# Optimization experiments

Hardware: AMD Instinct MI355X
Metric: run time of the kernel (lower is better)

The kernel has to match this reference:

```python
import jax, jax.numpy as jnp
import numpy as np

EPS = 1e-5

def layernorm(x, g, b):
    mu = jnp.mean(x, axis=-1, keepdims=True)
    var = jnp.mean((x - mu) ** 2, axis=-1, keepdims=True)
    return (x - mu) * jax.lax.rsqrt(var + EPS) * g + b

def setup_inputs() -> dict:
    key = jax.random.key(0)
    B, T, C, H = 4, 2048, 1024, 16
    hs = C // H  # 64
    ks = jax.random.split(key, 16)
    s_in = 1.0 / np.sqrt(C)
    s_hid = 1.0 / np.sqrt(4 * C)
    return {
        "x":   jax.random.normal(ks[0], (B, T, C), jnp.float32),
        # per-head projections, stacked over heads: [H, C, hs]
        "Wq":  jax.random.normal(ks[1], (H, C, hs), jnp.float32) * s_in,
        "Wk":  jax.random.normal(ks[2], (H, C, hs), jnp.float32) * s_in,
        "Wv":  jax.random.normal(ks[3], (H, C, hs), jnp.float32) * s_in,
        # output projection [C, C] (concat of heads -> C)
        "Wo":  jax.random.normal(ks[4], (C, C), jnp.float32) * s_in,
        "bo":  jnp.zeros((C,), jnp.float32),
        # layernorm params
        "g1":  jnp.ones((C,), jnp.float32),
        "be1": jnp.zeros((C,), jnp.float32),
        "g2":  jnp.ones((C,), jnp.float32),
        "be2": jnp.zeros((C,), jnp.float32),
        # feed-forward: C -> 4C -> C
        "W1":  jax.random.normal(ks[5], (C, 4 * C), jnp.float32) * s_in,
        "b1":  jnp.zeros((4 * C,), jnp.float32),
        "W2":  jax.random.normal(ks[6], (4 * C, C), jnp.float32) * s_hid,
        "b2":  jnp.zeros((C,), jnp.float32),
    }

def reference(x, Wq, Wk, Wv, Wo, bo, g1, be1, g2, be2, W1, b1, W2, b2):
    B, T, C = x.shape
    H, _, hs = Wq.shape
    scale = hs ** -0.5

    # --- self-attention on ln1(x) ---
    xn = layernorm(x, g1, be1)
    q = jnp.einsum('btc,hcd->bhtd', xn, Wq)
    k = jnp.einsum('btc,hcd->bhtd', xn, Wk)
    v = jnp.einsum('btc,hcd->bhtd', xn, Wv)
    scores = jnp.einsum('bhtd,bhsd->bhts', q, k) * scale  # [B,H,T,T]
    causal = jnp.tril(jnp.ones((T, T), dtype=bool))
    scores = jnp.where(causal, scores, jnp.finfo(scores.dtype).min)
    wei = jax.nn.softmax(scores, axis=-1)
    out = jnp.einsum('bhts,bhsd->bhtd', wei, v)           # [B,H,T,hs]
    out = out.transpose(0, 2, 1, 3).reshape(B, T, H * hs)  # concat heads
    x = x + out @ Wo + bo

    # --- feed-forward on ln2(x) ---
    xn2 = layernorm(x, g2, be2)
    h = jax.nn.relu(xn2 @ W1 + b1)
    x = x + h @ W2 + b2
    return x
```

## Files before the change

### kernel.cpp

```cpp
#include <hip/hip_runtime.h>
#include <hip/hip_bf16.h>

typedef __hip_bfloat16 bf16;
typedef __attribute__((ext_vector_type(8))) short bf16x8;
typedef __attribute__((ext_vector_type(4))) short s16x4;
typedef __attribute__((ext_vector_type(4))) float f32x4;
typedef __attribute__((ext_vector_type(16))) float f32x16;
typedef __attribute__((ext_vector_type(2))) unsigned int u32x2;
typedef __attribute__((ext_vector_type(4))) unsigned int u32x4;

__device__ __forceinline__ float b2f(bf16 v) { return __bfloat162float(v); }
__device__ __forceinline__ bf16  f2b(float v) { return __float2bfloat16(v); }
__device__ __forceinline__ float ldf(const bf16* p)  { return __bfloat162float(*p); }
__device__ __forceinline__ float ldf(const float* p) { return *p; }
__device__ __forceinline__ void  stf(bf16* p, float v)  { *p = __float2bfloat16(v); }
__device__ __forceinline__ void  stf(float* p, float v) { *p = v; }

__device__ __forceinline__ unsigned cvt_pk_bf16(float lo, float hi) {
    unsigned r;
    asm("v_cvt_pk_bf16_f32 %0, %1, %2" : "=v"(r) : "v"(lo), "v"(hi));
    return r;
}

__device__ __forceinline__ void ld4(const float* p, float* v) {
    float4 t = *(const float4*)p;
    v[0] = t.x; v[1] = t.y; v[2] = t.z; v[3] = t.w;
}
__device__ __forceinline__ void ld4(const bf16* p, float* v) {
    s16x4 t = *(const s16x4*)p;
#pragma unroll
    for (int j = 0; j < 4; ++j) { short s = t[j]; v[j] = b2f(*(bf16*)&s); }
}

__device__ __forceinline__ void load_lds16(const bf16* g, short* lds) {
    __builtin_amdgcn_global_load_lds(
        (const __attribute__((address_space(1))) unsigned int*)g,
        (__attribute__((address_space(3))) unsigned int*)lds, 16, 0, 0);
}

template<typename InT>
__global__ __launch_bounds__(256) void ln_kernel(const InT* __restrict__ x,
                                                 const float* __restrict__ g,
                                                 const float* __restrict__ b,
                                                 bf16* __restrict__ out)
{
    const int C = 1024;
    int row = blockIdx.x;
    int tid = threadIdx.x;
    const InT* xr = x + (size_t)row * C;

    float v[4];
    ld4(xr + tid * 4, v);
    float s = 0.f, s2 = 0.f;
#pragma unroll
    for (int i = 0; i < 4; ++i) { s += v[i]; s2 += v[i] * v[i]; }
#pragma unroll
    for (int off = 32; off > 0; off >>= 1) {
        s  += __shfl_down(s,  off, 64);
        s2 += __shfl_down(s2, off, 64);
    }
    __shared__ float red[8];
    int wave = tid >> 6;
    if ((tid & 63) == 0) { red[wave] = s; red[wave + 4] = s2; }
    __syncthreads();
    float ts  = red[0] + red[1] + red[2] + red[3];
    float ts2 = red[4] + red[5] + red[6] + red[7];
    float mu  = ts * (1.f / 1024.f);
    float var = ts2 * (1.f / 1024.f) - mu * mu;
    float rstd = rsqrtf(var + 1e-5f);

    float4 gg = *(const float4*)(g + tid * 4);
    float4 bb = *(const float4*)(b + tid * 4);
    float gj[4] = {gg.x, gg.y, gg.z, gg.w};
    float bj[4] = {bb.x, bb.y, bb.z, bb.w};
    s16x4 o4;
#pragma unroll
    for (int j = 0; j < 4; ++j) {
        bf16 ob = f2b((v[j] - mu) * rstd * gj[j] + bj[j]);
        o4[j] = *(short*)&ob;
    }
    *(s16x4*)(out + (size_t)row * C + tid * 4) = o4;
}

__global__ __launch_bounds__(256) void prep_weights(
    const float* __restrict__ Wq, const float* __restrict__ Wk,
    const float* __restrict__ Wv, const float* __restrict__ Wo,
    const float* __restrict__ W1, const float* __restrict__ W2,
    bf16* __restrict__ wqkvt, bf16* __restrict__ wot,
    bf16* __restrict__ w1t, bf16* __restrict__ w2t)
{
    __shared__ float t[32][33];
    int tx = threadIdx.x & 31, ty = threadIdx.x >> 5;
    int id = blockIdx.x;
    const float* in; bf16* out; int in_ld, out_ld, n0, k0;
    if (id < 3072) {
        const float* Ws[3] = {Wq, Wk, Wv};
        int m = id >> 10, r = id & 1023;
        int z = r >> 6, rt = r & 63;
        in = Ws[m] + z * 65536;
        out = wqkvt + (size_t)(m * 1024 + z * 64) * 1024;
        in_ld = 64; out_ld = 1024;
        n0 = (rt & 1) * 32; k0 = (rt >> 1) * 32;
    } else if (id < 4096) {
        int r = id - 3072;
        in = Wo; out = wot; in_ld = 1024; out_ld = 1024;
        n0 = (r & 31) * 32; k0 = (r >> 5) * 32;
    } else if (id < 8192) {
        int r = id - 4096;
        in = W1; out = w1t; in_ld = 4096; out_ld = 1024;
        n0 = (r & 127) * 32; k0 = (r >> 7) * 32;
    } else {
        int r = id - 8192;
        in = W2; out = w2t; in_ld = 1024; out_ld = 4096;
        n0 = (r & 31) * 32; k0 = (r >> 5) * 32;
    }
#pragma unroll
    for (int i = 0; i < 4; ++i)
        t[ty + i * 8][tx] = in[(size_t)(k0 + ty + i * 8) * in_ld + n0 + tx];
    __syncthreads();
#pragma unroll
    for (int i = 0; i < 4; ++i)
        out[(size_t)(n0 + ty + i * 8) * out_ld + k0 + tx] = f2b(t[tx][ty + i * 8]);
}

__global__ __launch_bounds__(256) void vt_kernel(
    const bf16* __restrict__ qkv, bf16* __restrict__ vt, int T)
{
    __shared__ float t[32][33];
    int tx = threadIdx.x & 31, ty = threadIdx.x >> 5;
    int z = blockIdx.z, b = z >> 4, h = z & 15;
    const bf16* in = qkv + (size_t)b * T * 3072 + 2048 + h * 64;
    bf16* out = vt + (size_t)z * 64 * T;
    int n0 = blockIdx.x * 32, k0 = blockIdx.y * 32;
#pragma unroll
    for (int i = 0; i < 4; ++i)
        t[ty + i * 8][tx] = b2f(in[(size_t)(k0 + ty + i * 8) * 3072 + n0 + tx]);
    __syncthreads();
#pragma unroll
    for (int i = 0; i < 4; ++i)
        out[(size_t)(n0 + ty + i * 8) * T + k0 + tx] = f2b(t[tx][ty + i * 8]);
}

template<bool RELU, bool HAS_BIAS, typename OutT>
__global__ __launch_bounds__(512, 2) void gemm8p(
    const bf16* __restrict__ A, int lda,
    const bf16* __restrict__ Bt, int ldb,
    const float* __restrict__ bias,
    OutT* __restrict__ Cm, int ldc,
    int M, int N, int K)
{
    __shared__ short As[4][8192];
    __shared__ short Bs[4][8192];
    int tid = threadIdx.x, wv = tid >> 6, ln = tid & 63;
    int quad = ln >> 4, lane15 = ln & 15;

    int nbn = N >> 8;
    int nwg = gridDim.x;
    int f2 = (blockIdx.x & 7) * (nwg >> 3) + (blockIdx.x >> 3);
    int by = f2 / nbn, bx = f2 % nbn;
    int bm0 = by << 8, bn0 = bx << 8;

    int wr = wv >> 2, wc = wv & 3;
    const int NT = K >> 5;

    int sr = tid >> 2;
    int sc = ((tid & 3) ^ ((sr >> 1) & 3)) * 8;
    const bf16* Ab1 = A  + (size_t)(bm0 + sr) * lda + sc;
    const bf16* Ab2 = A  + (size_t)(bm0 + 128 + sr) * lda + sc;
    const bf16* Bb1 = Bt + (size_t)(bn0 + sr) * ldb + sc;
    const bf16* Bb2 = Bt + (size_t)(bn0 + 128 + sr) * ldb + sc;

#define STAGE_A8(bf_, u_) { \
    load_lds16(Ab1 + (u_) * 32, &As[bf_][wv * 512]); \
    load_lds16(Ab2 + (u_) * 32, &As[bf_][4096 + wv * 512]); }
#define STAGE_B8(bf_, u_) { \
    load_lds16(Bb1 + (u_) * 32, &Bs[bf_][wv * 512]); \
    load_lds16(Bb2 + (u_) * 32, &Bs[bf_][4096 + wv * 512]); }

    f32x4 acc[8][4] = {};
    int arow = wr * 128 + lane15;
    int brow = wc * 64 + lane15;
    int sw = (quad ^ ((lane15 >> 1) & 3)) * 8;

    STAGE_A8(0, 0); STAGE_B8(0, 0);
    STAGE_A8(1, 1); STAGE_B8(1, 1);
    STAGE_A8(2, 2); STAGE_B8(2, 2);
    asm volatile("s_waitcnt vmcnt(8)" ::: "memory");
    __builtin_amdgcn_s_barrier();

    for (int t = 0; t < NT; ++t) {
        int buf = t & 3;
        const short* Al = &As[buf][0];
        const short* Bl = &Bs[buf][0];

        bf16x8 af[4], bfr[4];
#pragma unroll
        for (int mi = 0; mi < 4; ++mi)
            af[mi] = *(const bf16x8*)&Al[(arow + mi * 16) * 32 + sw];
#pragma unroll
        for (int ni = 0; ni < 4; ++ni)
            bfr[ni] = *(const bf16x8*)&Bl[(brow + ni * 16) * 32 + sw];
        if (t + 3 < NT) STAGE_A8((t + 3) & 3, t + 3);
        __builtin_amdgcn_s_barrier();
        __builtin_amdgcn_s_setprio(1);
#pragma unroll
        for (int mi = 0; mi < 4; ++mi)
#pragma unroll
            for (int ni = 0; ni < 4; ++ni)
                acc[mi][ni] = __builtin_amdgcn_mfma_f32_16x16x32_bf16(
                    af[mi], bfr[ni], acc[mi][ni], 0, 0, 0);
        __builtin_amdgcn_s_setprio(0);
        __builtin_amdgcn_s_barrier();

        bf16x8 ag[4];
#pragma unroll
        for (int mi = 0; mi < 4; ++mi)
            ag[mi] = *(const bf16x8*)&Al[(arow + (mi + 4) * 16) * 32 + sw];
        if (t + 3 < NT) STAGE_B8((t + 3) & 3, t + 3);
        if (t < NT - 3) {
            asm volatile("s_waitcnt vmcnt(8)" ::: "memory");
        } else if (t == NT - 3) {
            asm volatile("s_waitcnt vmcnt(4)" ::: "memory");
        } else if (t == NT - 2) {
            asm volatile("s_waitcnt vmcnt(0)" ::: "memory");
        }
        __builtin_amdgcn_s_barrier();
        __builtin_amdgcn_s_setprio(1);
#pragma unroll
        for (int mi = 0; mi < 4; ++mi)
#pragma unroll
            for (int ni = 0; ni < 4; ++ni)
                acc[mi + 4][ni] = __builtin_amdgcn_mfma_f32_16x16x32_bf16(
                    ag[mi], bfr[ni], acc[mi + 4][ni], 0, 0, 0);
        __builtin_amdgcn_s_setprio(0);
        __builtin_amdgcn_s_barrier();
    }

#undef STAGE_A8
#undef STAGE_B8

#pragma unroll
    for (int mi = 0; mi < 8; ++mi) {
#pragma unroll
        for (int r = 0; r < 4; ++r) {
            int gm = bm0 + wr * 128 + mi * 16 + quad * 4 + r;
#pragma unroll
            for (int ni = 0; ni < 4; ++ni) {
                int gn = bn0 + wc * 64 + ni * 16 + lane15;
                float v = acc[mi][ni][r];
                if (HAS_BIAS) v += bias[gn];
                if (RELU)     v = fmaxf(v, 0.f);
                stf(Cm + (size_t)gm * ldc + gn, v);
            }
        }
    }
}

template<int BK, bool RELU, bool HAS_BIAS, bool HAS_RES, typename ResT, typename OutT>
__global__ __launch_bounds__(256) void gemm_bt(
    const bf16* __restrict__ A, int lda,
    const bf16* __restrict__ Bt, int ldb,
    const float* __restrict__ bias,
    const ResT* __restrict__ res, int ldr,
    OutT* __restrict__ Cm, int ldc,
    int M, int N, int K)
{
    __shared__ short As[2][128 * BK];
    __shared__ short Bs[2][128 * BK];
    int tid = threadIdx.x, wv = tid >> 6, ln = tid & 63;

    int f = blockIdx.x + blockIdx.y * gridDim.x;
    int nby = gridDim.y;
    int by = f % nby, bx = f / nby;
    int bm0 = by * 128, bn0 = bx * 128;

    int wm = (wv & 1) * 64, wn = (wv >> 1) * 64;
    int quad = ln >> 4, lane15 = ln & 15;

    f32x4 acc[4][4] = {};

    const bf16* Ab = A + (size_t)bm0 * lda;
    const bf16* Bb = Bt + (size_t)bn0 * ldb;

    auto stage = [&](int buf, int kk) {
        if constexpr (BK == 32) {
            int srow = ln >> 2;
            int scol = (((ln & 3) ^ ((ln >> 3) & 3)) * 8);
#pragma unroll
            for (int i = 0; i < 2; ++i) {
                int ch = wv + i * 4;
                load_lds16(Ab + (size_t)(ch * 16 + srow) * lda + kk + scol,
                           &As[buf][ch * 16 * 32]);
                load_lds16(Bb + (size_t)(ch * 16 + srow) * ldb + kk + scol,
                           &Bs[buf][ch * 16 * 32]);
            }
        } else {
            int srow = ln >> 3;
            int scol = ((ln & 7) ^ srow) * 8;
#pragma unroll
            for (int i = 0; i < 4; ++i) {
                int r0 = i * 32 + wv * 8;
                load_lds16(Ab + (size_t)(r0 + srow) * lda + kk + scol,
                           &As[buf][r0 * 64]);
                load_lds16(Bb + (size_t)(r0 + srow) * ldb + kk + scol,
                           &Bs[buf][r0 * 64]);
            }
        }
    };

    stage(0, 0);
    __syncthreads();

    int cur = 0;
    for (int k0 = 0; k0 < K; k0 += BK) {
        if (k0 + BK < K) stage(cur ^ 1, k0 + BK);
        if constexpr (BK == 32) {
            int sw = (quad ^ ((lane15 >> 1) & 3)) * 8;
            bf16x8 af[4], bfr[4];
#pragma unroll
            for (int mi = 0; mi < 4; ++mi)
                af[mi] = *(const bf16x8*)&As[cur][(wm + mi * 16 + lane15) * 32 + sw];
#pragma unroll
            for (int ni = 0; ni < 4; ++ni)
                bfr[ni] = *(const bf16x8*)&Bs[cur][(wn + ni * 16 + lane15) * 32 + sw];
#pragma unroll
            for (int mi = 0; mi < 4; ++mi)
#pragma unroll
                for (int ni = 0; ni < 4; ++ni)
                    acc[mi][ni] = __builtin_amdgcn_mfma_f32_16x16x32_bf16(
                        af[mi], bfr[ni], acc[mi][ni], 0, 0, 0);
        } else {
#pragma unroll
            for (int ks = 0; ks < 2; ++ks) {
                int sw = (((ks * 4 + quad) ^ (lane15 & 7)) * 8);
                bf16x8 af[4], bfr[4];
#pragma unroll
                for (int mi = 0; mi < 4; ++mi)
                    af[mi] = *(const bf16x8*)&As[cur][(wm + mi * 16 + lane15) * 64 + sw];
#pragma unroll
                for (int ni = 0; ni < 4; ++ni)
                    bfr[ni] = *(const bf16x8*)&Bs[cur][(wn + ni * 16 + lane15) * 64 + sw];
#pragma unroll
                for (int mi = 0; mi < 4; ++mi)
#pragma unroll
                    for (int ni = 0; ni < 4; ++ni)
                        acc[mi][ni] = __builtin_amdgcn_mfma_f32_16x16x32_bf16(
                            af[mi], bfr[ni], acc[mi][ni], 0, 0, 0);
            }
        }
        __syncthreads();
        cur ^= 1;
    }

#pragma unroll
    for (int mi = 0; mi < 4; ++mi) {
#pragma unroll
        for (int r = 0; r < 4; ++r) {
            int gm = bm0 + wm + mi * 16 + quad * 4 + r;
#pragma unroll
            for (int ni = 0; ni < 4; ++ni) {
                int gn = bn0 + wn + ni * 16 + lane15;
                float v = acc[mi][ni][r];
                if (HAS_BIAS) v += bias[gn];
                if (HAS_RES)  v += ldf(res + (size_t)gm * ldr + gn);
                if (RELU)     v = fmaxf(v, 0.f);
                stf(Cm + (size_t)gm * ldc + gn, v);
            }
        }
    }
}

template<bool DUAL>
__device__ __forceinline__ void attn_tile32(
    const short* __restrict__ Ks, const short* __restrict__ Vs,
    const bf16x8* qfa, const bf16x8* qfb,
    f32x16* oa, f32x16* ob, float& lra, float& lrb,
    int kb, int qmina, int qminb, int l31, int hi, int l7)
{
    const float scale2 = 0.18033688011112042f;
    f32x16 sa[2] = {};
    f32x16 sb[2] = {};

    __builtin_amdgcn_s_setprio(1);
#pragma unroll
    for (int ts = 0; ts < 2; ++ts) {
#pragma unroll
        for (int ks = 0; ks < 4; ++ks) {
            bf16x8 kf = *(const bf16x8*)&Ks[(ts * 32 + l31) * 64 + (((ks * 2 + hi) ^ l7) * 8)];
            sa[ts] = __builtin_amdgcn_mfma_f32_32x32x16_bf16(kf, qfa[ks], sa[ts], 0, 0, 0);
            if (DUAL)
                sb[ts] = __builtin_amdgcn_mfma_f32_32x32x16_bf16(kf, qfb[ks], sb[ts], 0, 0, 0);
        }
    }
    __builtin_amdgcn_s_setprio(0);

    int qmin = DUAL ? qminb : qmina;
    if (kb + 63 > qmin) {
        int qcap = qmin + l31;
#pragma unroll
        for (int ts = 0; ts < 2; ++ts)
#pragma unroll
            for (int r = 0; r < 16; ++r) {
                int key = kb + ts * 32 + (r & 3) + 8 * (r >> 2) + 4 * hi;
                if (key > qcap) {
                    if (DUAL) sb[ts][r] = -3e38f; else sa[ts][r] = -3e38f;
                }
            }
    }

    float psa = 0.f, psb = 0.f;
#pragma unroll
    for (int ts = 0; ts < 2; ++ts)
#pragma unroll
        for (int r = 0; r < 16; ++r) {
            float va = exp2f(sa[ts][r] * scale2);
            sa[ts][r] = va; psa += va;
            if (DUAL) {
                float vb = exp2f(sb[ts][r] * scale2);
                sb[ts][r] = vb; psb += vb;
            }
        }
    lra += psa;
    if (DUAL) lrb += psb;

    __builtin_amdgcn_s_setprio(1);
#pragma unroll
    for (int s = 0; s < 4; ++s) {
        const int ts = s >> 1, q0 = (s & 1) * 8;
        unsigned a0 = cvt_pk_bf16(sa[ts][q0 + 0], sa[ts][q0 + 1]);
        unsigned a1 = cvt_pk_bf16(sa[ts][q0 + 2], sa[ts][q0 + 3]);
        unsigned a2 = cvt_pk_bf16(sa[ts][q0 + 4], sa[ts][q0 + 5]);
        unsigned a3 = cvt_pk_bf16(sa[ts][q0 + 6], sa[ts][q0 + 7]);
        u32x2 s02 = __builtin_amdgcn_permlane32_swap(a0, a2, false, false);
        u32x2 s13 = __builtin_amdgcn_permlane32_swap(a1, a3, false, false);
        u32x4 fa = {s02[0], s13[0], s02[1], s13[1]};
        bf16x8 pfa = *(bf16x8*)&fa;
        bf16x8 pfb;
        if (DUAL) {
            unsigned b0 = cvt_pk_bf16(sb[ts][q0 + 0], sb[ts][q0 + 1]);
            unsigned b1 = cvt_pk_bf16(sb[ts][q0 + 2], sb[ts][q0 + 3]);
            unsigned b2 = cvt_pk_bf16(sb[ts][q0 + 4], sb[ts][q0 + 5]);
            unsigned b3 = cvt_pk_bf16(sb[ts][q0 + 6], sb[ts][q0 + 7]);
            u32x2 t02 = __builtin_amdgcn_permlane32_swap(b0, b2, false, false);
            u32x2 t13 = __builtin_amdgcn_permlane32_swap(b1, b3, false, false);
            u32x4 fb = {t02[0], t13[0], t02[1], t13[1]};
            pfb = *(bf16x8*)&fb;
        }
#pragma unroll
        for (int dt = 0; dt < 2; ++dt) {
            bf16x8 vf = *(const bf16x8*)&Vs[(dt * 32 + l31) * 64 + (((s * 2 + hi) ^ l7) * 8)];
            oa[dt] = __builtin_amdgcn_mfma_f32_32x32x16_bf16(vf, pfa, oa[dt], 0, 0, 0);
            if (DUAL)
                ob[dt] = __builtin_amdgcn_mfma_f32_32x32x16_bf16(vf, pfb, ob[dt], 0, 0, 0);
        }
    }
    __builtin_amdgcn_s_setprio(0);
}

__global__ __launch_bounds__(512, 2) void attn_kernel(
    const bf16* __restrict__ qkv, const bf16* __restrict__ vt,
    bf16* __restrict__ o, int T)
{
    const int LDQ = 3072;
    int bx = blockIdx.x;
    int qta = 7 - bx;
    int qtb = bx;
    int h = blockIdx.y, b = blockIdx.z;
    int tid = threadIdx.x, wv = tid >> 6, ln = tid & 63;
    int l31 = ln & 31, hi = ln >> 5, l7 = ln & 7;

    __shared__ short KV[2][2][64 * 64];

    int lr = ln >> 3;
    int lc = ((ln & 7) ^ lr) * 8;

    const bf16* kbase = qkv + (size_t)(b * T) * LDQ + 1024 + h * 64;
    const bf16* vbase = vt + (size_t)((b * 16 + h) * 64) * T;

    bf16x8 qfa[4], qfb[4];
    {
        const bf16* qa = qkv + (size_t)(b * T + qta * 256 + wv * 32 + l31) * LDQ + h * 64 + hi * 8;
        const bf16* qb = qkv + (size_t)(b * T + qtb * 256 + wv * 32 + l31) * LDQ + h * 64 + hi * 8;
#pragma unroll
        for (int ks = 0; ks < 4; ++ks) {
            qfa[ks] = *(const bf16x8*)(qa + ks * 16);
            qfb[ks] = *(const bf16x8*)(qb + ks * 16);
        }
    }

    f32x16 oa[2] = {}, ob[2] = {};
    float lra = 0.f, lrb = 0.f;
    int qmina = qta * 256 + wv * 32;
    int qminb = qtb * 256 + wv * 32;
    int ntiles = (qta + 1) * 4;

    const bf16* kp = kbase + (size_t)(wv * 8 + lr) * LDQ + lc;
    const bf16* vp = vbase + (size_t)(wv * 8 + lr) * T + lc;
    load_lds16(kp, &KV[0][0][wv * 8 * 64]);
    load_lds16(vp, &KV[0][1][wv * 8 * 64]);

    for (int kt = 0; kt < ntiles; ++kt) {
        __syncthreads();
        if (kt + 1 < ntiles) {
            int nb = (kt + 1) & 1;
            kp += 64 * LDQ;
            vp += 64;
            load_lds16(kp, &KV[nb][0][wv * 8 * 64]);
            load_lds16(vp, &KV[nb][1][wv * 8 * 64]);
        }
        const short* Ks = &KV[kt & 1][0][0];
        const short* Vs = &KV[kt & 1][1][0];
        int kb = kt * 64;

        if (kb <= qminb + 31)
            attn_tile32<true>(Ks, Vs, qfa, qfb, oa, ob, lra, lrb,
                              kb, qmina, qminb, l31, hi, l7);
        else if (kb <= qmina + 31)
            attn_tile32<false>(Ks, Vs, qfa, qfb, oa, ob, lra, lrb,
                               kb, qmina, qminb, l31, hi, l7);
    }

    lra += __shfl_xor(lra, 32, 64);
    float inva = 1.f / lra;
    size_t rowa = (size_t)(b * T + qta * 256 + wv * 32 + l31);
#pragma unroll
    for (int dt = 0; dt < 2; ++dt)
#pragma unroll
        for (int rq = 0; rq < 4; ++rq) {
            u32x2 ou;
            ou[0] = cvt_pk_bf16(oa[dt][rq * 4 + 0] * inva, oa[dt][rq * 4 + 1] * inva);
            ou[1] = cvt_pk_bf16(oa[dt][rq * 4 + 2] * inva, oa[dt][rq * 4 + 3] * inva);
            *(u32x2*)&o[rowa * 1024 + h * 64 + dt * 32 + rq * 8 + hi * 4] = ou;
        }

    lrb += __shfl_xor(lrb, 32, 64);
    float invb = 1.f / lrb;
    size_t rowb = (size_t)(b * T + qtb * 256 + wv * 32 + l31);
#pragma unroll
    for (int dt = 0; dt < 2; ++dt)
#pragma unroll
        for (int rq = 0; rq < 4; ++rq) {
            u32x2 ou;
            ou[0] = cvt_pk_bf16(ob[dt][rq * 4 + 0] * invb, ob[dt][rq * 4 + 1] * invb);
            ou[1] = cvt_pk_bf16(ob[dt][rq * 4 + 2] * invb, ob[dt][rq * 4 + 3] * invb);
            *(u32x2*)&o[rowb * 1024 + h * 64 + dt * 32 + rq * 8 + hi * 4] = ou;
        }
}

extern "C" void kernel_launch(void* const* d_in, const int* in_sizes, int n_in,
                              void* d_out, int out_size, void* d_ws, size_t ws_size,
                              hipStream_t stream)
{
    (void)in_sizes; (void)n_in; (void)out_size; (void)ws_size;
    const float* x   = (const float*)d_in[0];
    const float* Wq  = (const float*)d_in[1];
    const float* Wk  = (const float*)d_in[2];
    const float* Wv  = (const float*)d_in[3];
    const float* Wo  = (const float*)d_in[4];
    const float* bo  = (const float*)d_in[5];
    const float* g1  = (const float*)d_in[6];
    const float* be1 = (const float*)d_in[7];
    const float* g2  = (const float*)d_in[8];
    const float* be2 = (const float*)d_in[9];
    const float* W1  = (const float*)d_in[10];
    const float* b1  = (const float*)d_in[11];
    const float* W2  = (const float*)d_in[12];
    const float* b2  = (const float*)d_in[13];

    const int T = 2048, M = 4 * T;
    const size_t MB = 1ull << 20;
    char* ws = (char*)d_ws;

    bf16*  xn    = (bf16*)(ws + 0 * MB);
    bf16*  qkv   = (bf16*)(ws + 16 * MB);
    bf16*  vt    = (bf16*)(ws + 64 * MB);
    bf16*  wqkvt = (bf16*)(ws + 80 * MB);
    bf16*  x1b   = (bf16*)(ws + 80 * MB);
    bf16*  wot   = (bf16*)(ws + 96 * MB);
    bf16*  xn2   = (bf16*)(ws + 96 * MB);
    bf16*  w1t   = (bf16*)(ws + 112 * MB);
    bf16*  w2t   = (bf16*)(ws + 120 * MB);
    bf16*  attnb = (bf16*)(ws + 0 * MB);
    bf16*  hb    = (bf16*)(ws + 0 * MB);

    dim3 blk(256);

    prep_weights<<<12288, blk, 0, stream>>>(Wq, Wk, Wv, Wo, W1, W2,
                                            wqkvt, wot, w1t, w2t);

    ln_kernel<float><<<M, blk, 0, stream>>>(x, g1, be1, xn);

    gemm8p<false, false, bf16><<<dim3(384), dim3(512), 0, stream>>>(
        xn, 1024, wqkvt, 1024, nullptr, qkv, 3072, M, 3072, 1024);

    vt_kernel<<<dim3(2, T / 32, 64), blk, 0, stream>>>(qkv, vt, T);

    attn_kernel<<<dim3(4, 16, 4), dim3(512), 0, stream>>>(qkv, vt, attnb, T);

    gemm_bt<32, false, true, true, float, bf16><<<dim3(8, 64), blk, 0, stream>>>(
        attnb, 1024, wot, 1024, bo, x, 1024, x1b, 1024, M, 1024, 1024);

    ln_kernel<bf16><<<M, blk, 0, stream>>>(x1b, g2, be2, xn2);

    gemm8p<true, true, bf16><<<dim3(512), dim3(512), 0, stream>>>(
        xn2, 1024, w1t, 1024, b1, hb, 4096, M, 4096, 1024);

    gemm_bt<64, false, true, true, bf16, float><<<dim3(8, 64), blk, 0, stream>>>(
        hb, 4096, w2t, 4096, b2, x1b, 1024, (float*)d_out, 1024, M, 1024, 4096);
}
```

Measured before the change: 485.8 us.

## Fuse V transpose into QKV GEMM epilogue and merge GEMM K-loop halves

Removes the separate vt_kernel launch. The QKV GEMM epilogue now writes the transposed V slice straight to the vt buffer as packed bf16 pairs, which saves one kernel launch and a full read and write of V. The main loop is also restructured to load all 8 A fragments at once, issue the A and B prefetch together, and run the 32 MFMAs in a single phase per iteration instead of two. That halves the number of barriers per K step, but it raises register pressure and reduces the interleaving of loads with MFMAs.

```diff
diff --git a/kernel.cpp b/kernel.cpp
--- a/kernel.cpp
+++ b/kernel.cpp
@@ -123,30 +123,13 @@
         out[(size_t)(n0 + ty + i * 8) * out_ld + k0 + tx] = f2b(t[tx][ty + i * 8]);
 }
 
-__global__ __launch_bounds__(256) void vt_kernel(
-    const bf16* __restrict__ qkv, bf16* __restrict__ vt, int T)
-{
-    __shared__ float t[32][33];
-    int tx = threadIdx.x & 31, ty = threadIdx.x >> 5;
-    int z = blockIdx.z, b = z >> 4, h = z & 15;
-    const bf16* in = qkv + (size_t)b * T * 3072 + 2048 + h * 64;
-    bf16* out = vt + (size_t)z * 64 * T;
-    int n0 = blockIdx.x * 32, k0 = blockIdx.y * 32;
-#pragma unroll
-    for (int i = 0; i < 4; ++i)
-        t[ty + i * 8][tx] = b2f(in[(size_t)(k0 + ty + i * 8) * 3072 + n0 + tx]);
-    __syncthreads();
-#pragma unroll
-    for (int i = 0; i < 4; ++i)
-        out[(size_t)(n0 + ty + i * 8) * T + k0 + tx] = f2b(t[tx][ty + i * 8]);
-}
-
-template<bool RELU, bool HAS_BIAS, typename OutT>
+template<bool RELU, bool HAS_BIAS, bool VSTORE, typename OutT>
 __global__ __launch_bounds__(512, 2) void gemm8p(
     const bf16* __restrict__ A, int lda,
     const bf16* __restrict__ Bt, int ldb,
     const float* __restrict__ bias,
     OutT* __restrict__ Cm, int ldc,
+    bf16* __restrict__ vt, int T,
     int M, int N, int K)
 {
     __shared__ short As[4][8192];
@@ -193,30 +176,14 @@
         const short* Al = &As[buf][0];
         const short* Bl = &Bs[buf][0];
 
-        bf16x8 af[4], bfr[4];
-#pragma unroll
-        for (int mi = 0; mi < 4; ++mi)
+        bf16x8 af[8], bfr[4];
+#pragma unroll
+        for (int mi = 0; mi < 8; ++mi)
             af[mi] = *(const bf16x8*)&Al[(arow + mi * 16) * 32 + sw];
 #pragma unroll
         for (int ni = 0; ni < 4; ++ni)
             bfr[ni] = *(const bf16x8*)&Bl[(brow + ni * 16) * 32 + sw];
-        if (t + 3 < NT) STAGE_A8((t + 3) & 3, t + 3);
-        __builtin_amdgcn_s_barrier();
-        __builtin_amdgcn_s_setprio(1);
-#pragma unroll
-        for (int mi = 0; mi < 4; ++mi)
-#pragma unroll
-            for (int ni = 0; ni < 4; ++ni)
-                acc[mi][ni] = __builtin_amdgcn_mfma_f32_16x16x32_bf16(
-                    af[mi], bfr[ni], acc[mi][ni], 0, 0, 0);
-        __builtin_amdgcn_s_setprio(0);
-        __builtin_amdgcn_s_barrier();
-
-        bf16x8 ag[4];
-#pragma unroll
-        for (int mi = 0; mi < 4; ++mi)
-            ag[mi] = *(const bf16x8*)&Al[(arow + (mi + 4) * 16) * 32 + sw];
-        if (t + 3 < NT) STAGE_B8((t + 3) & 3, t + 3);
+        if (t + 3 < NT) { STAGE_A8((t + 3) & 3, t + 3); STAGE_B8((t + 3) & 3, t + 3); }
         if (t < NT - 3) {
             asm volatile("s_waitcnt vmcnt(8)" ::: "memory");
         } else if (t == NT - 3) {
@@ -227,11 +194,11 @@
         __builtin_amdgcn_s_barrier();
         __builtin_amdgcn_s_setprio(1);
 #pragma unroll
-        for (int mi = 0; mi < 4; ++mi)
+        for (int mi = 0; mi < 8; ++mi)
 #pragma unroll
             for (int ni = 0; ni < 4; ++ni)
-                acc[mi + 4][ni] = __builtin_amdgcn_mfma_f32_16x16x32_bf16(
-                    ag[mi], bfr[ni], acc[mi + 4][ni], 0, 0, 0);
+                acc[mi][ni] = __builtin_amdgcn_mfma_f32_16x16x32_bf16(
+                    af[mi], bfr[ni], acc[mi][ni], 0, 0, 0);
         __builtin_amdgcn_s_setprio(0);
         __builtin_amdgcn_s_barrier();
     }
@@ -241,16 +208,26 @@
 
 #pragma unroll
     for (int mi = 0; mi < 8; ++mi) {
-#pragma unroll
-        for (int r = 0; r < 4; ++r) {
-            int gm = bm0 + wr * 128 + mi * 16 + quad * 4 + r;
-#pragma unroll
-            for (int ni = 0; ni < 4; ++ni) {
-                int gn = bn0 + wc * 64 + ni * 16 + lane15;
+        int gm0 = bm0 + wr * 128 + mi * 16 + quad * 4;
+#pragma unroll
+        for (int ni = 0; ni < 4; ++ni) {
+            int gn = bn0 + wc * 64 + ni * 16 + lane15;
+            float vv[4];
+#pragma unroll
+            for (int r = 0; r < 4; ++r) {
                 float v = acc[mi][ni][r];
                 if (HAS_BIAS) v += bias[gn];
                 if (RELU)     v = fmaxf(v, 0.f);
-                stf(Cm + (size_t)gm * ldc + gn, v);
+                vv[r] = v;
+                stf(Cm + (size_t)(gm0 + r) * ldc + gn, v);
+            }
+            if (VSTORE && gn >= 2048) {
+                int hd = gn - 2048;
+                int bb = gm0 >> 11, t0 = gm0 & 2047;
+                u32x2 pk;
+                pk[0] = cvt_pk_bf16(vv[0], vv[1]);
+                pk[1] = cvt_pk_bf16(vv[2], vv[3]);
+                *(u32x2*)&vt[(size_t)(bb * 1024 + hd) * T + t0] = pk;
             }
         }
     }
@@ -590,10 +567,8 @@
 
     ln_kernel<float><<<M, blk, 0, stream>>>(x, g1, be1, xn);
 
-    gemm8p<false, false, bf16><<<dim3(384), dim3(512), 0, stream>>>(
-        xn, 1024, wqkvt, 1024, nullptr, qkv, 3072, M, 3072, 1024);
-
-    vt_kernel<<<dim3(2, T / 32, 64), blk, 0, stream>>>(qkv, vt, T);
+    gemm8p<false, false, true, bf16><<<dim3(384), dim3(512), 0, stream>>>(
+        xn, 1024, wqkvt, 1024, nullptr, qkv, 3072, vt, T, M, 3072, 1024);
 
     attn_kernel<<<dim3(4, 16, 4), dim3(512), 0, stream>>>(qkv, vt, attnb, T);
 
@@ -602,8 +577,8 @@
 
     ln_kernel<bf16><<<M, blk, 0, stream>>>(x1b, g2, be2, xn2);
 
-    gemm8p<true, true, bf16><<<dim3(512), dim3(512), 0, stream>>>(
-        xn2, 1024, w1t, 1024, b1, hb, 4096, M, 4096, 1024);
+    gemm8p<true, true, false, bf16><<<dim3(512), dim3(512), 0, stream>>>(
+        xn2, 1024, w1t, 1024, b1, hb, 4096, nullptr, T, M, 4096, 1024);
 
     gemm_bt<64, false, true, true, bf16, float><<<dim3(8, 64), blk, 0, stream>>>(
         hb, 4096, w2t, 4096, b2, x1b, 1024, (float*)d_out, 1024, M, 1024, 4096);
```

Result: faster. 472.7 us (-2.7%).
